# Performance work log

Hardware: AMD Instinct MI355X
Metric: run time of the kernel (lower is better)

The kernel has to match this reference:

```python
import jax, jax.numpy as jnp
import numpy as np

N = 20000          # nodes
E = 320000         # edges (avg degree 16)
C0, C1, C2 = 128, 64, 32   # multiplicities of 0e,1e,2e in node embedding (dim 480)
FC = 64            # edge scalar feature dim (fc_neurons[0])
WN = 3 * C0        # depthwise TP weight numel for nonzero paths
AVG_AGG = 16.0
LN_EPS = 1e-5


def setup_inputs() -> dict:
    key = jax.random.key(0)
    ks = jax.random.split(key, 20)
    inp = {
        'node_input':   jax.random.normal(ks[0], (N, 480), jnp.float32),
        'edge_attr':    jax.random.normal(ks[1], (E, 9), jnp.float32),   # sh lmax=2
        'edge_scalars': jax.random.normal(ks[2], (E, FC), jnp.float32),
        'edge_src':     jax.random.randint(ks[3], (E,), 0, N),
        'edge_dst':     jax.random.randint(ks[4], (E,), 0, N),
        'batch':        jnp.zeros((N,), jnp.int32),
        # exp: LinearRS 1x0e -> 128x0e (bias on scalars)
        'exp_w':  jax.random.normal(ks[5], (C0,), jnp.float32),
        'exp_b':  jax.random.normal(ks[6], (C0,), jnp.float32) * 0.1,
        # radial MLP: 64 -> 64 (LN, SiLU) -> 384
        'rad_w1': jax.random.normal(ks[7], (FC, FC), jnp.float32) / np.sqrt(FC),
        'rad_b1': jnp.zeros((FC,), jnp.float32),
        'rad_gamma': jnp.ones((FC,), jnp.float32),
        'rad_beta':  jnp.zeros((FC,), jnp.float32),
        'rad_w2': jax.random.normal(ks[8], (FC, WN), jnp.float32) / np.sqrt(FC),
        'rad_b2': jnp.zeros((WN,), jnp.float32),
        'proj_w0': jax.random.normal(ks[9], (C0, C0), jnp.float32) / np.sqrt(C0),
        'proj_b0': jnp.zeros((C0,), jnp.float32),
        'proj_w1': jax.random.normal(ks[10], (C0, C1), jnp.float32) / np.sqrt(C0),
        'proj_w2': jax.random.normal(ks[11], (C0, C2), jnp.float32) / np.sqrt(C0),
    }
    return inp


def reference(node_input, edge_attr, edge_scalars, edge_src, edge_dst, batch,
              exp_w, exp_b, rad_w1, rad_b1, rad_gamma, rad_beta, rad_w2, rad_b2,
              proj_w0, proj_b0, proj_w1, proj_w2):
    n = node_input.shape[0]
    # exp: ones -> 128x0e scalars (l>0 outputs of a scalar->irreps linear are zero)
    ones = jnp.ones_like(node_input[:, :1])            # [N,1]
    node_scal = ones * exp_w[None, :] + exp_b          # [N,128]
    # radial profile: Linear -> LayerNorm -> SiLU -> Linear
    h = edge_scalars @ rad_w1 + rad_b1
    mu = h.mean(-1, keepdims=True)
    var = h.var(-1, keepdims=True)
    h = (h - mu) * jax.lax.rsqrt(var + LN_EPS) * rad_gamma + rad_beta
    h = jax.nn.silu(h)
    w = (h @ rad_w2 + rad_b2).reshape(-1, 3, C0)       # [E,3,128] per-path dw weights
    # gather source node scalars
    s = node_scal[edge_src]                            # [E,128]
    sh0 = edge_attr[:, 0:1]                            # [E,1]
    sh1 = edge_attr[:, 1:4]                            # [E,3]
    sh2 = edge_attr[:, 4:9]                            # [E,5]
    # depthwise tensor product: 0e (x) l -> l (CG is identity up to norm)
    out0 = (s * w[:, 0]) * sh0                         # [E,128]
    out1 = (s * w[:, 1])[:, :, None] * sh1[:, None, :] # [E,128,3]
    out2 = (s * w[:, 2])[:, :, None] * sh2[:, None, :] # [E,128,5]
    # equivariant projection per degree
    y0 = out0 @ proj_w0 + proj_b0                      # [E,128]
    y1 = jnp.einsum('ecm,cd->edm', out1, proj_w1)      # [E,64,3]
    y2 = jnp.einsum('ecm,cd->edm', out2, proj_w2)      # [E,32,5]
    y = jnp.concatenate([y0, y1.reshape(-1, C1 * 3), y2.reshape(-1, C2 * 5)], axis=-1)  # [E,480]
    # scaled scatter-add to destination nodes
    agg = jax.ops.segment_sum(y, edge_dst, num_segments=n)
    return agg / jnp.sqrt(jnp.asarray(AVG_AGG, y.dtype))
```

## Files before the change

kernel.cpp:

```cpp
#include <hip/hip_runtime.h>

#define FCn 64
#define LDP 68
#define TEB 64
#define GJK 576
#define GJS 612
#define ABP 12
#define ZBLK 512

__device__ __forceinline__ float silu_f(float x) { return x / (1.f + __expf(-x)); }

__global__ __launch_bounds__(256) void precomp_kernel(
    const float* __restrict__ exp_w, const float* __restrict__ exp_b,
    const float* __restrict__ rad_w2, const float* __restrict__ rad_b2,
    const float* __restrict__ proj_w0, const float* __restrict__ proj_b0,
    const float* __restrict__ proj_w1, const float* __restrict__ proj_w2,
    float* __restrict__ MT, float* __restrict__ cvec, float* __restrict__ b0s,
    float* __restrict__ zbase, long long zf4, int* __restrict__ cnt, int Nn)
{
    if (blockIdx.x >= 65) {
        const long long tid = (long long)(blockIdx.x - 65) * 256 + threadIdx.x;
        const long long stride = (long long)ZBLK * 256;
        float4 z = make_float4(0.f, 0.f, 0.f, 0.f);
        for (long long i = tid; i < zf4; i += stride) ((float4*)zbase)[i] = z;
        for (long long i = tid; i < Nn; i += stride) cnt[i] = 0;
        return;
    }
    const int r = blockIdx.x;
    const int c = threadIdx.x;
    const float* wrow = (r < FCn) ? (rad_w2 + (long long)r * 384) : rad_b2;
    float acc = 0.f;
    if (c < 128) {
        for (int q = 0; q < 128; ++q)
            acc += wrow[q] * (exp_w[q] + exp_b[q]) * proj_w0[q * 128 + c];
    } else if (c < 192) {
        const int d = c - 128;
        for (int q = 0; q < 128; ++q)
            acc += wrow[128 + q] * (exp_w[q] + exp_b[q]) * proj_w1[q * 64 + d];
    } else if (c < 224) {
        const int d = c - 192;
        for (int q = 0; q < 128; ++q)
            acc += wrow[256 + q] * (exp_w[q] + exp_b[q]) * proj_w2[q * 32 + d];
    }
    acc *= 0.25f;
    if (r < FCn) {
        if (c < 224) MT[c * FCn + r] = acc;
    } else {
        cvec[c] = acc;
        if (c < 128) b0s[c] = 0.25f * proj_b0[c];
    }
}

__global__ __launch_bounds__(256) void hist_kernel(const int* __restrict__ dst, int* __restrict__ cnt, int E)
{
    for (int e = blockIdx.x * 256 + threadIdx.x; e < E; e += gridDim.x * 256)
        atomicAdd(&cnt[dst[e]], 1);
}

__global__ __launch_bounds__(256) void scan_kernel(const int* __restrict__ cnt, int* __restrict__ off,
                                                   int* __restrict__ cur, int Nn, int Etot)
{
    __shared__ int part[256];
    __shared__ int spart[257];
    const int t = threadIdx.x;
    const int per = (Nn + 255) / 256;
    int s = 0;
    #pragma unroll 8
    for (int i = 0; i < per; ++i) {
        const int idx = t * per + i;
        if (idx < Nn) s += cnt[idx];
    }
    part[t] = s;
    __syncthreads();
    if (t == 0) {
        int run = 0;
        spart[0] = 0;
        for (int i = 0; i < 256; ++i) { run += part[i]; spart[i + 1] = run; }
    }
    __syncthreads();
    int run = spart[t];
    #pragma unroll 8
    for (int i = 0; i < per; ++i) {
        const int idx = t * per + i;
        if (idx < Nn) { off[idx] = run; cur[idx] = run; run += cnt[idx]; }
    }
    if (t == 0) off[Nn] = Etot;
}

__global__ __launch_bounds__(256) void scatter_kernel(const int* __restrict__ dst, int* __restrict__ cur,
                                                      int* __restrict__ eids, int E)
{
    for (int e = blockIdx.x * 256 + threadIdx.x; e < E; e += gridDim.x * 256) {
        const int pos = atomicAdd(&cur[dst[e]], 1);
        eids[pos] = e;
    }
}

__global__ __launch_bounds__(256, 7) void accumG_kernel(
    const float* __restrict__ edge_attr,
    const float* __restrict__ edge_scalars,
    const int*   __restrict__ eids,
    const int*   __restrict__ edge_dst,
    const float* __restrict__ rad_w1,
    const float* __restrict__ rad_b1,
    const float* __restrict__ rad_gamma,
    const float* __restrict__ rad_beta,
    float* __restrict__ G,
    float* __restrict__ Ab,
    int E)
{
    __shared__ float XT[FCn * LDP];
    __shared__ float Ea[TEB * ABP];
    __shared__ int   dst_l[TEB];
    const int t = threadIdx.x;
    const int p0 = blockIdx.x * TEB;

    if (t < TEB) {
        const int p = p0 + t;
        const int eid = (p < E) ? eids[p] : -1;
        dst_l[t] = (eid >= 0) ? edge_dst[eid] : -1;
    }

    #pragma unroll
    for (int i = 0; i < 4; ++i) {
        const int idx = i * 256 + t;
        const int e  = idx >> 4;
        const int kq = idx & 15;
        const int p  = p0 + e;
        const int eid = (p < E) ? eids[p] : -1;
        float4 v = make_float4(0.f, 0.f, 0.f, 0.f);
        if (eid >= 0) v = *(const float4*)(edge_scalars + (long long)eid * FCn + kq * 4);
        XT[(kq * 4 + 0) * LDP + e] = v.x;
        XT[(kq * 4 + 1) * LDP + e] = v.y;
        XT[(kq * 4 + 2) * LDP + e] = v.z;
        XT[(kq * 4 + 3) * LDP + e] = v.w;
    }
    for (int i = t; i < TEB * 9; i += 256) {
        const int e = i / 9, j = i - e * 9;
        const int p = p0 + e;
        const int eid = (p < E) ? eids[p] : -1;
        Ea[e * ABP + j] = (eid >= 0) ? edge_attr[(long long)eid * 9 + j] : 0.f;
    }
    __syncthreads();

    const int eg = t >> 4, cg = t & 15;
    float a[4][4];
    #pragma unroll
    for (int i = 0; i < 4; ++i)
        #pragma unroll
        for (int j = 0; j < 4; ++j) a[i][j] = 0.f;
    for (int k = 0; k < FCn; ++k) {
        const float4 xv = *(const float4*)&XT[k * LDP + eg * 4];
        const float4 wv = *(const float4*)&rad_w1[k * FCn + cg * 4];
        const float xe[4] = {xv.x, xv.y, xv.z, xv.w};
        const float wc[4] = {wv.x, wv.y, wv.z, wv.w};
        #pragma unroll
        for (int i = 0; i < 4; ++i)
            #pragma unroll
            for (int j = 0; j < 4; ++j)
                a[i][j] += xe[i] * wc[j];
    }
    {
        const float4 bv = *(const float4*)&rad_b1[cg * 4];
        const float bb[4] = {bv.x, bv.y, bv.z, bv.w};
        #pragma unroll
        for (int i = 0; i < 4; ++i)
            #pragma unroll
            for (int j = 0; j < 4; ++j) a[i][j] += bb[j];
    }

    float s1[4], s2[4];
    #pragma unroll
    for (int i = 0; i < 4; ++i) {
        s1[i] = a[i][0] + a[i][1] + a[i][2] + a[i][3];
        s2[i] = a[i][0]*a[i][0] + a[i][1]*a[i][1] + a[i][2]*a[i][2] + a[i][3]*a[i][3];
    }
    #pragma unroll
    for (int m = 1; m < 16; m <<= 1) {
        #pragma unroll
        for (int i = 0; i < 4; ++i) {
            s1[i] += __shfl_xor(s1[i], m);
            s2[i] += __shfl_xor(s2[i], m);
        }
    }

    __syncthreads();

    {
        const float4 gm = *(const float4*)&rad_gamma[cg * 4];
        const float4 bt = *(const float4*)&rad_beta[cg * 4];
        const float gv[4] = {gm.x, gm.y, gm.z, gm.w};
        const float bv2[4] = {bt.x, bt.y, bt.z, bt.w};
        #pragma unroll
        for (int i = 0; i < 4; ++i) {
            const float mu  = s1[i] * (1.f / 64.f);
            const float var = s2[i] * (1.f / 64.f) - mu * mu;
            const float rs  = rsqrtf(var + 1e-5f);
            float o[4];
            #pragma unroll
            for (int j = 0; j < 4; ++j) {
                const float x = (a[i][j] - mu) * rs * gv[j] + bv2[j];
                o[j] = silu_f(x);
            }
            *(float4*)&XT[(eg * 4 + i) * LDP + cg * 4] = make_float4(o[0], o[1], o[2], o[3]);
        }
    }
    __syncthreads();

    const int k  = t & 63;
    const int jg = t >> 6;
    const int j0 = jg, j1 = jg + 4;
    const bool has2 = (jg == 0);
    float g0 = 0.f, g1 = 0.f, g2 = 0.f;
    float a0 = 0.f, a1 = 0.f, a2 = 0.f;
    int curn = dst_l[0];
    int e = 0;
    while (e < TEB) {
        const int nid = dst_l[e];
        if (nid != curn) {
            if (curn >= 0) {
                float* gp = G + (long long)curn * GJK;
                atomicAdd(gp + j0 * 64 + k, g0);
                atomicAdd(gp + j1 * 64 + k, g1);
                if (has2) atomicAdd(gp + 8 * 64 + k, g2);
                if (k == 0) {
                    float* ap = Ab + (long long)curn * ABP;
                    atomicAdd(ap + j0, a0);
                    atomicAdd(ap + j1, a1);
                    if (has2) atomicAdd(ap + 8, a2);
                }
            }
            g0 = g1 = g2 = 0.f; a0 = a1 = a2 = 0.f;
            curn = nid;
        }
        if (nid < 0) break;
        if (e + 4 <= TEB && dst_l[e + 3] == nid) {
            #pragma unroll
            for (int u = 0; u < 4; ++u) {
                const int eu = e + u;
                const float h  = XT[eu * LDP + k];
                const float e0 = Ea[eu * ABP + j0];
                const float e1 = Ea[eu * ABP + j1];
                g0 = fmaf(e0, h, g0); a0 += e0;
                g1 = fmaf(e1, h, g1); a1 += e1;
                if (has2) {
                    const float e2 = Ea[eu * ABP + 8];
                    g2 = fmaf(e2, h, g2); a2 += e2;
                }
            }
            e += 4;
        } else {
            const float h  = XT[e * LDP + k];
            const float e0 = Ea[e * ABP + j0];
            const float e1 = Ea[e * ABP + j1];
            g0 = fmaf(e0, h, g0); a0 += e0;
            g1 = fmaf(e1, h, g1); a1 += e1;
            if (has2) {
                const float e2 = Ea[e * ABP + 8];
                g2 = fmaf(e2, h, g2); a2 += e2;
            }
            e += 1;
        }
    }
    if (curn >= 0) {
        float* gp = G + (long long)curn * GJK;
        atomicAdd(gp + j0 * 64 + k, g0);
        atomicAdd(gp + j1 * 64 + k, g1);
        if (has2) atomicAdd(gp + 8 * 64 + k, g2);
        if (k == 0) {
            float* ap = Ab + (long long)curn * ABP;
            atomicAdd(ap + j0, a0);
            atomicAdd(ap + j1, a1);
            if (has2) atomicAdd(ap + 8, a2);
        }
    }
}

__global__ __launch_bounds__(512) void project_kernel(
    const float* __restrict__ G, const float* __restrict__ Ab,
    const int*   __restrict__ off,
    const float* __restrict__ MT, const float* __restrict__ cvec,
    const float* __restrict__ b0s,
    float* __restrict__ out, int Nn)
{
    __shared__ float Gs[8 * GJS];
    const int t = threadIdx.x;

    int tIdx = 0, jIdx = 0;
    if (t < 128)      { tIdx = t; jIdx = 0; }
    else if (t < 320) { const int idx = t - 128; tIdx = 128 + idx / 3; jIdx = 1 + idx % 3; }
    else if (t < 480) { const int idx = t - 320; tIdx = 192 + idx / 5; jIdx = 4 + idx % 5; }

    const int n0b = blockIdx.x * 8;

    for (int i = t; i < 8 * 144; i += 512) {
        const int nb  = i / 144;
        const int rem = i - nb * 144;
        const int n   = n0b + nb;
        float4 v = make_float4(0.f, 0.f, 0.f, 0.f);
        if (n < Nn) v = *(const float4*)(G + (long long)n * GJK + rem * 4);
        *(float4*)(&Gs[nb * GJS + (rem >> 4) * 68 + (rem & 15) * 4]) = v;
    }

    float4 m[16];
    {
        const float* mrow = MT + tIdx * FCn;
        #pragma unroll
        for (int q = 0; q < 16; ++q) m[q] = *(const float4*)(mrow + q * 4);
    }
    const float cvv = cvec[tIdx];
    const float bsv = (t < 128) ? b0s[t] : 0.f;
    __syncthreads();

    #pragma unroll 1
    for (int g = 0; g < 2; ++g) {
        const int n0 = n0b + g * 4;
        if (n0 >= Nn) break;

        float acc[4];
        #pragma unroll
        for (int nb = 0; nb < 4; ++nb) {
            const int n = min(n0 + nb, Nn - 1);
            const int deg = off[n + 1] - off[n];
            acc[nb] = Ab[(long long)n * ABP + jIdx] * cvv + (float)deg * bsv;
        }
        const float* gb = &Gs[(g * 4) * GJS + jIdx * 68];
        #pragma unroll
        for (int q = 0; q < 16; ++q) {
            const float4 mq = m[q];
            #pragma unroll
            for (int nb = 0; nb < 4; ++nb) {
                const float4 gv = *(const float4*)(gb + nb * GJS + q * 4);
                acc[nb] += mq.x * gv.x + mq.y * gv.y + mq.z * gv.z + mq.w * gv.w;
            }
        }
        if (t < 480) {
            #pragma unroll
            for (int nb = 0; nb < 4; ++nb)
                if (n0 + nb < Nn)
                    out[(long long)(n0 + nb) * 480 + t] = acc[nb];
        }
    }
}

extern "C" void kernel_launch(void* const* d_in, const int* in_sizes, int n_in,
                              void* d_out, int out_size, void* d_ws, size_t ws_size,
                              hipStream_t stream)
{
    const float* edge_attr    = (const float*)d_in[1];
    const float* edge_scalars = (const float*)d_in[2];
    const int*   edge_dst     = (const int*)d_in[4];
    const float* exp_w     = (const float*)d_in[6];
    const float* exp_b     = (const float*)d_in[7];
    const float* rad_w1    = (const float*)d_in[8];
    const float* rad_b1    = (const float*)d_in[9];
    const float* rad_gamma = (const float*)d_in[10];
    const float* rad_beta  = (const float*)d_in[11];
    const float* rad_w2    = (const float*)d_in[12];
    const float* rad_b2    = (const float*)d_in[13];
    const float* proj_w0   = (const float*)d_in[14];
    const float* proj_b0   = (const float*)d_in[15];
    const float* proj_w1   = (const float*)d_in[16];
    const float* proj_w2   = (const float*)d_in[17];
    float* out = (float*)d_out;
    const int E = in_sizes[4];
    const int Nn = out_size / 480;

    float* MT   = (float*)d_ws;
    float* cvec = MT + 224 * FCn;
    float* b0s  = cvec + 256;
    int* off  = (int*)(b0s + 128);
    int* cnt  = off + (Nn + 1);
    int* cur  = cnt + Nn;
    int* eids = cur + Nn;
    size_t gOff = (size_t)((char*)(eids + E) - (char*)d_ws);
    gOff = (gOff + 255) & ~(size_t)255;
    float* G  = (float*)((char*)d_ws + gOff);
    float* Ab = G + (size_t)Nn * GJK;

    const long long zf4 = ((long long)Nn * (GJK + ABP)) >> 2;
    precomp_kernel<<<65 + ZBLK, 256, 0, stream>>>(exp_w, exp_b, rad_w2, rad_b2,
                                                  proj_w0, proj_b0, proj_w1, proj_w2,
                                                  MT, cvec, b0s, G, zf4, cnt, Nn);
    hist_kernel<<<512, 256, 0, stream>>>(edge_dst, cnt, E);
    scan_kernel<<<1, 256, 0, stream>>>(cnt, off, cur, Nn, E);
    scatter_kernel<<<512, 256, 0, stream>>>(edge_dst, cur, eids, E);

    const int blocks = (E + TEB - 1) / TEB;
    accumG_kernel<<<blocks, 256, 0, stream>>>(edge_attr, edge_scalars, eids, edge_dst,
                                              rad_w1, rad_b1, rad_gamma, rad_beta,
                                              G, Ab, E);
    const int pblocks = (Nn + 7) / 8;
    project_kernel<<<pblocks, 512, 0, stream>>>(G, Ab, off, MT, cvec, b0s, out, Nn);
}
```

Measured before the change: 466.0 us.

## Swizzle accumG shared layout, widen edge unroll, and double project nodes per block

Replaces the padded transposed shared-memory layout in accumG with an XOR-swizzled layout to reduce bank conflicts, and packs edge attributes at stride 9 instead of 12. It also adds an 8-edge unrolled accumulation path and raises the occupancy hint from 7 to 8 waves. The project kernel now handles 16 nodes per block instead of 8, amortizing per-thread weight-row loads over more nodes. The trade-offs are more register pressure under the higher occupancy hint and double the LDS per project block, which may lower its occupancy.

```diff
diff --git a/kernel.cpp b/kernel.cpp
--- a/kernel.cpp
+++ b/kernel.cpp
@@ -1,14 +1,17 @@
 #include <hip/hip_runtime.h>
 
 #define FCn 64
-#define LDP 68
 #define TEB 64
 #define GJK 576
 #define GJS 612
 #define ABP 12
 #define ZBLK 512
+#define XSZ (64*68)
 
 __device__ __forceinline__ float silu_f(float x) { return x / (1.f + __expf(-x)); }
+__device__ __forceinline__ int xidx(int r, int c) {
+    return r * 68 + (c ^ (((r >> 3) & 7) << 2));
+}
 
 __global__ __launch_bounds__(256) void precomp_kernel(
     const float* __restrict__ exp_w, const float* __restrict__ exp_b,
@@ -96,7 +99,7 @@
     }
 }
 
-__global__ __launch_bounds__(256, 7) void accumG_kernel(
+__global__ __launch_bounds__(256, 8) void accumG_kernel(
     const float* __restrict__ edge_attr,
     const float* __restrict__ edge_scalars,
     const int*   __restrict__ eids,
@@ -109,8 +112,8 @@
     float* __restrict__ Ab,
     int E)
 {
-    __shared__ float XT[FCn * LDP];
-    __shared__ float Ea[TEB * ABP];
+    __shared__ float XT[XSZ];
+    __shared__ float Ea[TEB * 9];
     __shared__ int   dst_l[TEB];
     const int t = threadIdx.x;
     const int p0 = blockIdx.x * TEB;
@@ -130,16 +133,18 @@
         const int eid = (p < E) ? eids[p] : -1;
         float4 v = make_float4(0.f, 0.f, 0.f, 0.f);
         if (eid >= 0) v = *(const float4*)(edge_scalars + (long long)eid * FCn + kq * 4);
-        XT[(kq * 4 + 0) * LDP + e] = v.x;
-        XT[(kq * 4 + 1) * LDP + e] = v.y;
-        XT[(kq * 4 + 2) * LDP + e] = v.z;
-        XT[(kq * 4 + 3) * LDP + e] = v.w;
+        const int ec = e ^ (((kq >> 1) & 7) << 2);
+        const int b0 = (kq * 4) * 68 + ec;
+        XT[b0       ] = v.x;
+        XT[b0 + 68  ] = v.y;
+        XT[b0 + 136 ] = v.z;
+        XT[b0 + 204 ] = v.w;
     }
     for (int i = t; i < TEB * 9; i += 256) {
         const int e = i / 9, j = i - e * 9;
         const int p = p0 + e;
         const int eid = (p < E) ? eids[p] : -1;
-        Ea[e * ABP + j] = (eid >= 0) ? edge_attr[(long long)eid * 9 + j] : 0.f;
+        Ea[i] = (eid >= 0) ? edge_attr[(long long)eid * 9 + j] : 0.f;
     }
     __syncthreads();
 
@@ -149,8 +154,9 @@
     for (int i = 0; i < 4; ++i)
         #pragma unroll
         for (int j = 0; j < 4; ++j) a[i][j] = 0.f;
+    #pragma unroll 2
     for (int k = 0; k < FCn; ++k) {
-        const float4 xv = *(const float4*)&XT[k * LDP + eg * 4];
+        const float4 xv = *(const float4*)&XT[xidx(k, eg * 4)];
         const float4 wv = *(const float4*)&rad_w1[k * FCn + cg * 4];
         const float xe[4] = {xv.x, xv.y, xv.z, xv.w};
         const float wc[4] = {wv.x, wv.y, wv.z, wv.w};
@@ -202,7 +208,7 @@
                 const float x = (a[i][j] - mu) * rs * gv[j] + bv2[j];
                 o[j] = silu_f(x);
             }
-            *(float4*)&XT[(eg * 4 + i) * LDP + cg * 4] = make_float4(o[0], o[1], o[2], o[3]);
+            *(float4*)&XT[xidx(eg * 4 + i, cg * 4)] = make_float4(o[0], o[1], o[2], o[3]);
         }
     }
     __syncthreads();
@@ -234,29 +240,44 @@
             curn = nid;
         }
         if (nid < 0) break;
-        if (e + 4 <= TEB && dst_l[e + 3] == nid) {
-            #pragma unroll
-            for (int u = 0; u < 4; ++u) {
+        if (e + 8 <= TEB && dst_l[e + 7] == nid) {
+            #pragma unroll
+            for (int u = 0; u < 8; ++u) {
                 const int eu = e + u;
-                const float h  = XT[eu * LDP + k];
-                const float e0 = Ea[eu * ABP + j0];
-                const float e1 = Ea[eu * ABP + j1];
+                const float h  = XT[xidx(eu, k)];
+                const float e0 = Ea[eu * 9 + j0];
+                const float e1 = Ea[eu * 9 + j1];
                 g0 = fmaf(e0, h, g0); a0 += e0;
                 g1 = fmaf(e1, h, g1); a1 += e1;
                 if (has2) {
-                    const float e2 = Ea[eu * ABP + 8];
+                    const float e2 = Ea[eu * 9 + 8];
                     g2 = fmaf(e2, h, g2); a2 += e2;
                 }
             }
+            e += 8;
+        } else if (e + 4 <= TEB && dst_l[e + 3] == nid) {
+            #pragma unroll
+            for (int u = 0; u < 4; ++u) {
+                const int eu = e + u;
+                const float h  = XT[xidx(eu, k)];
+                const float e0 = Ea[eu * 9 + j0];
+                const float e1 = Ea[eu * 9 + j1];
+                g0 = fmaf(e0, h, g0); a0 += e0;
+                g1 = fmaf(e1, h, g1); a1 += e1;
+                if (has2) {
+                    const float e2 = Ea[eu * 9 + 8];
+                    g2 = fmaf(e2, h, g2); a2 += e2;
+                }
+            }
             e += 4;
         } else {
-            const float h  = XT[e * LDP + k];
-            const float e0 = Ea[e * ABP + j0];
-            const float e1 = Ea[e * ABP + j1];
+            const float h  = XT[xidx(e, k)];
+            const float e0 = Ea[e * 9 + j0];
+            const float e1 = Ea[e * 9 + j1];
             g0 = fmaf(e0, h, g0); a0 += e0;
             g1 = fmaf(e1, h, g1); a1 += e1;
             if (has2) {
-                const float e2 = Ea[e * ABP + 8];
+                const float e2 = Ea[e * 9 + 8];
                 g2 = fmaf(e2, h, g2); a2 += e2;
             }
             e += 1;
@@ -283,7 +304,7 @@
     const float* __restrict__ b0s,
     float* __restrict__ out, int Nn)
 {
-    __shared__ float Gs[8 * GJS];
+    __shared__ float Gs[16 * GJS];
     const int t = threadIdx.x;
 
     int tIdx = 0, jIdx = 0;
@@ -291,9 +312,9 @@
     else if (t < 320) { const int idx = t - 128; tIdx = 128 + idx / 3; jIdx = 1 + idx % 3; }
     else if (t < 480) { const int idx = t - 320; tIdx = 192 + idx / 5; jIdx = 4 + idx % 5; }
 
-    const int n0b = blockIdx.x * 8;
-
-    for (int i = t; i < 8 * 144; i += 512) {
+    const int n0b = blockIdx.x * 16;
+
+    for (int i = t; i < 16 * 144; i += 512) {
         const int nb  = i / 144;
         const int rem = i - nb * 144;
         const int n   = n0b + nb;
@@ -313,7 +334,7 @@
     __syncthreads();
 
     #pragma unroll 1
-    for (int g = 0; g < 2; ++g) {
+    for (int g = 0; g < 4; ++g) {
         const int n0 = n0b + g * 4;
         if (n0 >= Nn) break;
 
@@ -390,6 +411,6 @@
     accumG_kernel<<<blocks, 256, 0, stream>>>(edge_attr, edge_scalars, eids, edge_dst,
                                               rad_w1, rad_b1, rad_gamma, rad_beta,
                                               G, Ab, E);
-    const int pblocks = (Nn + 7) / 8;
+    const int pblocks = (Nn + 15) / 16;
     project_kernel<<<pblocks, 512, 0, stream>>>(G, Ab, off, MT, cvec, b0s, out, Nn);
 }
```

After: 464.1 us. Within noise of the previous version (-0.4%).
